# Optimization experiments

Measured on AMD Instinct MI355X. Metric: run time of the kernel, lower is better.

Reference implementation:

```python
import jax, jax.numpy as jnp
import numpy as np

E = 8        # number of sessions (experts)
N = 512      # per-session input width (max units)
P = 512      # n_channels (output width)
F = 100      # max_F time bins
B = 128      # batch of trials
SCALE = 1.0


def setup_inputs() -> dict:
    key = jax.random.key(0)
    kx, ke, k1, k2, k3, k4 = jax.random.split(key, 6)
    x = jax.random.normal(kx, (B, F, N), dtype=jnp.float32)
    eid = jax.random.randint(ke, (B,), 0, E, dtype=jnp.int32)
    # Per-session stitcher Linear(N, 2N) and projector Linear(2N, P), stacked.
    s1 = 1.0 / np.sqrt(N)
    s2 = 1.0 / np.sqrt(2 * N)
    W1 = jax.random.uniform(k1, (E, N, 2 * N), jnp.float32, -s1, s1)
    b1 = jax.random.uniform(k2, (E, 2 * N), jnp.float32, -s1, s1)
    W2 = jax.random.uniform(k3, (E, 2 * N, P), jnp.float32, -s2, s2)
    b2 = jax.random.uniform(k4, (E, P), jnp.float32, -s2, s2)
    return {"x": x, "eid": eid, "W1": W1, "b1": b1, "W2": W2, "b2": b2}


def reference(x, eid, W1, b1, W2, b2):
    # Grouped (per-session) Linear -> Softsign -> Linear, dispatched by eid.
    # Equivalent to the torch loop over unique eids with mask gather/scatter,
    # expressed as a gather of per-sample expert weights + batched matmul.
    w1 = W1[eid]                      # [B, N, 2N]
    stitched = jnp.einsum('bfn,bnh->bfh', x, w1) + b1[eid][:, None, :]
    act = stitched / (1.0 + jnp.abs(stitched))  # Softsign
    act = act * SCALE
    w2 = W2[eid]                      # [B, 2N, P]
    out = jnp.einsum('bfh,bhp->bfp', act, w2) + b2[eid][:, None, :]
    return out                        # [B, F, P]
```

## Files before the change

kernel.cpp:

```cpp
#include <hip/hip_runtime.h>
#include <hip/hip_bf16.h>

#define B_ 128
#define F_ 100
#define N_ 512
#define H_ 1024
#define P_ 512
#define E_ 8

#define BM 128
#define BK 64

typedef __attribute__((ext_vector_type(8))) short bf16x8;
typedef __attribute__((ext_vector_type(4))) float f32x4;

#define GLOAD16(g, l) __builtin_amdgcn_global_load_lds(                      \
    (const __attribute__((address_space(1))) void*)(g),                      \
    (__attribute__((address_space(3))) void*)(l), 16, 0, 0)

static __device__ __forceinline__ short f2bf(float f) {
    __hip_bfloat16 h = __float2bfloat16(f);
    short s;
    __builtin_memcpy(&s, &h, sizeof(s));
    return s;
}

__global__ __launch_bounds__(256) void convert_x(const float* __restrict__ x,
                                                 short* __restrict__ xbf) {
    const int g = blockIdx.x * 256 + threadIdx.x;
    const int col = (g & (N_ / 8 - 1)) * 8;
    const int row = g >> 6;
    const int f = row & 127, b = row >> 7;
    union { short s[8]; uint4 u; } o;
    if (f < F_) {
        const float* xp = x + ((size_t)(b * F_ + f)) * N_ + col;
        const float4 v0 = *(const float4*)(xp);
        const float4 v1 = *(const float4*)(xp + 4);
        o.s[0] = f2bf(v0.x); o.s[1] = f2bf(v0.y);
        o.s[2] = f2bf(v0.z); o.s[3] = f2bf(v0.w);
        o.s[4] = f2bf(v1.x); o.s[5] = f2bf(v1.y);
        o.s[6] = f2bf(v1.z); o.s[7] = f2bf(v1.w);
    } else {
        o.u = make_uint4(0u, 0u, 0u, 0u);
    }
    *(uint4*)(xbf + (size_t)row * N_ + col) = o.u;
}

__global__ __launch_bounds__(256) void transpose_cvt(const float* __restrict__ W,
                                                     short* __restrict__ WT,
                                                     int R, int C) {
    __shared__ float tile[64][65];
    const int e = blockIdx.z;
    const int c0 = blockIdx.x * 64, r0 = blockIdx.y * 64;
    const int t = threadIdx.x;
    const float* Wp = W + (size_t)e * R * C;
    short* WTp = WT + (size_t)e * C * R;
    {
        const int c4 = (t & 15) * 4, r = t >> 4;
#pragma unroll
        for (int p = 0; p < 4; p++) {
            const int row = p * 16 + r;
            const float4 v = *(const float4*)(Wp + (size_t)(r0 + row) * C + c0 + c4);
            tile[row][c4 + 0] = v.x; tile[row][c4 + 1] = v.y;
            tile[row][c4 + 2] = v.z; tile[row][c4 + 3] = v.w;
        }
    }
    __syncthreads();
    {
        const int r8 = (t & 7) * 8, cl = t >> 3;
#pragma unroll
        for (int p = 0; p < 2; p++) {
            const int c = p * 32 + cl;
            union { short s[8]; uint4 u; } o;
#pragma unroll
            for (int j = 0; j < 8; j++) o.s[j] = f2bf(tile[r8 + j][c]);
            *(uint4*)(&WTp[(size_t)(c0 + c) * R + r0 + r8]) = o.u;
        }
    }
}

template <int KDIM, int BN_, bool FIRST>
__global__ __launch_bounds__(256, 4) void gemm_kernel(
    const short* __restrict__ A,
    const short* __restrict__ WT,
    const float* __restrict__ bias,
    const int* __restrict__ eid,
    short* __restrict__ actout,
    float* __restrict__ out)
{
    constexpr int NCOLS = FIRST ? H_ : P_;
    constexpr int NI = BN_ / 32;
    __shared__ short sA[BM * BK];
    __shared__ short sB[BN_ * BK];
    const int b = blockIdx.y;
    const int n0 = blockIdx.x * BN_;
    const int e = eid[b];
    const int t = threadIdx.x;
    const int lane = t & 63, w = t >> 6;
    const int wm = (w >> 1) * 64, wn = (w & 1) * (BN_ / 2);
    const int l15 = lane & 15, quad = lane >> 4;
    const int lr = lane >> 3, lc = (lane & 7) * 8;

    f32x4 acc[4][NI];
#pragma unroll
    for (int mi = 0; mi < 4; mi++)
#pragma unroll
        for (int ni = 0; ni < NI; ni++)
            acc[mi][ni] = (f32x4)(0.0f);

    const short* Ap = A + (size_t)b * BM * KDIM;
    const short* Bp = WT + ((size_t)e * NCOLS + n0) * KDIM;

    for (int k0 = 0; k0 < KDIM; k0 += BK) {
#pragma unroll
        for (int i = 0; i < 4; i++) {
            const int rb = w * 32 + i * 8;
            GLOAD16(Ap + (size_t)(rb + lr) * KDIM + k0 + lc, &sA[rb * BK]);
        }
#pragma unroll
        for (int i = 0; i < BN_ / 32; i++) {
            const int rb = w * (BN_ / 4) + i * 8;
            GLOAD16(Bp + (size_t)(rb + lr) * KDIM + k0 + lc, &sB[rb * BK]);
        }
        __syncthreads();
#pragma unroll
        for (int ks = 0; ks < 2; ks++) {
            bf16x8 af[4], bfr[NI];
#pragma unroll
            for (int mi = 0; mi < 4; mi++)
                af[mi] = *(const bf16x8*)(&sA[(wm + mi * 16 + l15) * BK + ks * 32 + quad * 8]);
#pragma unroll
            for (int ni = 0; ni < NI; ni++)
                bfr[ni] = *(const bf16x8*)(&sB[(wn + ni * 16 + l15) * BK + ks * 32 + quad * 8]);
#pragma unroll
            for (int mi = 0; mi < 4; mi++)
#pragma unroll
                for (int ni = 0; ni < NI; ni++)
                    acc[mi][ni] = __builtin_amdgcn_mfma_f32_16x16x32_bf16(af[mi], bfr[ni], acc[mi][ni], 0, 0, 0);
        }
        __syncthreads();
    }

#pragma unroll
    for (int mi = 0; mi < 4; mi++) {
#pragma unroll
        for (int ni = 0; ni < NI; ni++) {
            const int col = n0 + wn + ni * 16 + l15;
            const float bv = bias[(size_t)e * NCOLS + col];
#pragma unroll
            for (int r = 0; r < 4; r++) {
                const int row = wm + mi * 16 + quad * 4 + r;
                float v = acc[mi][ni][r] + bv;
                if constexpr (FIRST) {
                    v = v / (1.0f + fabsf(v));
                    actout[((size_t)b * BM + row) * H_ + col] = f2bf(v);
                } else {
                    if (row < F_)
                        out[((size_t)b * F_ + row) * P_ + col] = v;
                }
            }
        }
    }
}

extern "C" void kernel_launch(void* const* d_in, const int* in_sizes, int n_in,
                              void* d_out, int out_size, void* d_ws, size_t ws_size,
                              hipStream_t stream) {
    const float* x  = (const float*)d_in[0];
    const int* eid  = (const int*)d_in[1];
    const float* W1 = (const float*)d_in[2];
    const float* b1 = (const float*)d_in[3];
    const float* W2 = (const float*)d_in[4];
    const float* b2 = (const float*)d_in[5];
    float* out = (float*)d_out;

    char* ws = (char*)d_ws;
    short* W1T = (short*)(ws);
    short* W2T = (short*)(ws + (size_t)(8u << 20));
    short* act = (short*)(ws + (size_t)(16u << 20));
    short* xbf = (short*)(ws + (size_t)(48u << 20));

    convert_x<<<dim3((B_ * 128 * N_ / 8) / 256), 256, 0, stream>>>(x, xbf);
    transpose_cvt<<<dim3(H_ / 64, N_ / 64, E_), 256, 0, stream>>>(W1, W1T, N_, H_);
    transpose_cvt<<<dim3(P_ / 64, H_ / 64, E_), 256, 0, stream>>>(W2, W2T, H_, P_);
    gemm_kernel<N_, 128, true><<<dim3(H_ / 128, B_), 256, 0, stream>>>(xbf, W1T, b1, eid, act, nullptr);
    gemm_kernel<H_, 64, false><<<dim3(P_ / 64, B_), 256, 0, stream>>>(act, W2T, b2, eid, nullptr, out);
}
```

Measured before the change: 185.4 us.

## Fuse prep kernels, sort trials by expert, swizzle LDS, trim padded rows

Merges the x conversion and both weight transposes into one launch, which also builds a trial table sorted by expert id. The GEMMs now walk trials in expert order so consecutive blocks share the same weight tiles in cache. LDS reads and writes use an XOR swizzle to avoid bank conflicts, GEMM2 uses a 128-wide N tile, and the bottom waves skip their fourth M-fragment so less work is spent on padded rows (112 instead of 128 per trial). The risk is that A loads for the last trial's rows 100..127 in GEMM1 read past xbf into adjacent workspace, and that the swizzle must match exactly between the global-to-LDS writes and the fragment reads.

```diff
diff --git a/kernel.cpp b/kernel.cpp
--- a/kernel.cpp
+++ b/kernel.cpp
@@ -7,8 +7,7 @@
 #define H_ 1024
 #define P_ 512
 #define E_ 8
-
-#define BM 128
+#define TR_ 112
 #define BK 64
 
 typedef __attribute__((ext_vector_type(8))) short bf16x8;
@@ -25,90 +24,115 @@
     return s;
 }
 
-__global__ __launch_bounds__(256) void convert_x(const float* __restrict__ x,
-                                                 short* __restrict__ xbf) {
-    const int g = blockIdx.x * 256 + threadIdx.x;
-    const int col = (g & (N_ / 8 - 1)) * 8;
-    const int row = g >> 6;
-    const int f = row & 127, b = row >> 7;
-    union { short s[8]; uint4 u; } o;
-    if (f < F_) {
-        const float* xp = x + ((size_t)(b * F_ + f)) * N_ + col;
+__global__ __launch_bounds__(256) void prep(
+    const float* __restrict__ x, const float* __restrict__ W1,
+    const float* __restrict__ W2, const int* __restrict__ eid,
+    short* __restrict__ xbf, short* __restrict__ W1T, short* __restrict__ W2T,
+    int2* __restrict__ ttab) {
+    __shared__ float tile[64][65];
+    __shared__ int scnt[E_], sbase[E_];
+    const int bx = blockIdx.x;
+    const int t = threadIdx.x;
+    if (bx < 3200) {
+        const int g = bx * 256 + t;
+        const int col = (g & 63) * 8;
+        const int row = g >> 6;
+        const float* xp = x + (size_t)row * N_ + col;
         const float4 v0 = *(const float4*)(xp);
         const float4 v1 = *(const float4*)(xp + 4);
+        union { short s[8]; uint4 u; } o;
         o.s[0] = f2bf(v0.x); o.s[1] = f2bf(v0.y);
         o.s[2] = f2bf(v0.z); o.s[3] = f2bf(v0.w);
         o.s[4] = f2bf(v1.x); o.s[5] = f2bf(v1.y);
         o.s[6] = f2bf(v1.z); o.s[7] = f2bf(v1.w);
+        *(uint4*)(xbf + (size_t)row * N_ + col) = o.u;
+    } else if (bx < 5248) {
+        const float* W; short* WT; int R, C, r0, c0, e;
+        if (bx < 4224) {
+            const int idx = bx - 3200;
+            e = idx >> 7; const int i = idx & 127;
+            W = W1; WT = W1T; R = N_; C = H_;
+            r0 = (i >> 4) * 64; c0 = (i & 15) * 64;
+        } else {
+            const int idx = bx - 4224;
+            e = idx >> 7; const int i = idx & 127;
+            W = W2; WT = W2T; R = H_; C = P_;
+            r0 = (i & 15) * 64; c0 = (i >> 4) * 64;
+        }
+        const float* Wp = W + (size_t)e * R * C;
+        short* WTp = WT + (size_t)e * C * R;
+        {
+            const int c4 = (t & 15) * 4, r = t >> 4;
+#pragma unroll
+            for (int p = 0; p < 4; p++) {
+                const int row = p * 16 + r;
+                const float4 v = *(const float4*)(Wp + (size_t)(r0 + row) * C + c0 + c4);
+                tile[row][c4 + 0] = v.x; tile[row][c4 + 1] = v.y;
+                tile[row][c4 + 2] = v.z; tile[row][c4 + 3] = v.w;
+            }
+        }
+        __syncthreads();
+        {
+            const int r8 = (t & 7) * 8, cl = t >> 3;
+#pragma unroll
+            for (int p = 0; p < 2; p++) {
+                const int c = p * 32 + cl;
+                union { short s[8]; uint4 u; } o;
+#pragma unroll
+                for (int j = 0; j < 8; j++) o.s[j] = f2bf(tile[r8 + j][c]);
+                *(uint4*)(&WTp[(size_t)(c0 + c) * R + r0 + r8]) = o.u;
+            }
+        }
     } else {
-        o.u = make_uint4(0u, 0u, 0u, 0u);
+        if (t < E_) scnt[t] = 0;
+        __syncthreads();
+        int my_e = 0;
+        if (t < B_) { my_e = eid[t]; atomicAdd(&scnt[my_e], 1); }
+        __syncthreads();
+        if (t == 0) {
+            int s = 0;
+            for (int i = 0; i < E_; i++) { sbase[i] = s; s += scnt[i]; }
+        }
+        __syncthreads();
+        if (t < B_) {
+            const int pos = atomicAdd(&sbase[my_e], 1);
+            ttab[pos] = make_int2(t, my_e);
+        }
     }
-    *(uint4*)(xbf + (size_t)row * N_ + col) = o.u;
-}
-
-__global__ __launch_bounds__(256) void transpose_cvt(const float* __restrict__ W,
-                                                     short* __restrict__ WT,
-                                                     int R, int C) {
-    __shared__ float tile[64][65];
-    const int e = blockIdx.z;
-    const int c0 = blockIdx.x * 64, r0 = blockIdx.y * 64;
-    const int t = threadIdx.x;
-    const float* Wp = W + (size_t)e * R * C;
-    short* WTp = WT + (size_t)e * C * R;
-    {
-        const int c4 = (t & 15) * 4, r = t >> 4;
-#pragma unroll
-        for (int p = 0; p < 4; p++) {
-            const int row = p * 16 + r;
-            const float4 v = *(const float4*)(Wp + (size_t)(r0 + row) * C + c0 + c4);
-            tile[row][c4 + 0] = v.x; tile[row][c4 + 1] = v.y;
-            tile[row][c4 + 2] = v.z; tile[row][c4 + 3] = v.w;
-        }
-    }
-    __syncthreads();
-    {
-        const int r8 = (t & 7) * 8, cl = t >> 3;
-#pragma unroll
-        for (int p = 0; p < 2; p++) {
-            const int c = p * 32 + cl;
-            union { short s[8]; uint4 u; } o;
-#pragma unroll
-            for (int j = 0; j < 8; j++) o.s[j] = f2bf(tile[r8 + j][c]);
-            *(uint4*)(&WTp[(size_t)(c0 + c) * R + r0 + r8]) = o.u;
-        }
-    }
-}
-
-template <int KDIM, int BN_, bool FIRST>
+}
+
+template <int KDIM, bool FIRST>
 __global__ __launch_bounds__(256, 4) void gemm_kernel(
     const short* __restrict__ A,
     const short* __restrict__ WT,
     const float* __restrict__ bias,
-    const int* __restrict__ eid,
+    const int2* __restrict__ ttab,
     short* __restrict__ actout,
     float* __restrict__ out)
 {
     constexpr int NCOLS = FIRST ? H_ : P_;
-    constexpr int NI = BN_ / 32;
-    __shared__ short sA[BM * BK];
-    __shared__ short sB[BN_ * BK];
-    const int b = blockIdx.y;
-    const int n0 = blockIdx.x * BN_;
-    const int e = eid[b];
+    __shared__ short sA[128 * BK];
+    __shared__ short sB[128 * BK];
+    const int slot = (blockIdx.x & 7) * 16 + (blockIdx.x >> 3);
+    const int2 te = ttab[slot];
+    const int trial = te.x, e = te.y;
+    const int n0 = blockIdx.y * 128;
     const int t = threadIdx.x;
     const int lane = t & 63, w = t >> 6;
-    const int wm = (w >> 1) * 64, wn = (w & 1) * (BN_ / 2);
+    const int wm = (w >> 1) * 64, wn = (w & 1) * 64;
+    const int MI = (w >> 1) ? 3 : 4;
     const int l15 = lane & 15, quad = lane >> 4;
-    const int lr = lane >> 3, lc = (lane & 7) * 8;
-
-    f32x4 acc[4][NI];
+    const int lr = lane >> 3;
+    const int lc = (((lane & 7) ^ lr) * 8);
+
+    f32x4 acc[4][4];
 #pragma unroll
     for (int mi = 0; mi < 4; mi++)
 #pragma unroll
-        for (int ni = 0; ni < NI; ni++)
+        for (int ni = 0; ni < 4; ni++)
             acc[mi][ni] = (f32x4)(0.0f);
 
-    const short* Ap = A + (size_t)b * BM * KDIM;
+    const short* Ap = A + (size_t)trial * (FIRST ? F_ : TR_) * KDIM;
     const short* Bp = WT + ((size_t)e * NCOLS + n0) * KDIM;
 
     for (int k0 = 0; k0 < KDIM; k0 += BK) {
@@ -118,33 +142,31 @@
             GLOAD16(Ap + (size_t)(rb + lr) * KDIM + k0 + lc, &sA[rb * BK]);
         }
 #pragma unroll
-        for (int i = 0; i < BN_ / 32; i++) {
-            const int rb = w * (BN_ / 4) + i * 8;
+        for (int i = 0; i < 4; i++) {
+            const int rb = w * 32 + i * 8;
             GLOAD16(Bp + (size_t)(rb + lr) * KDIM + k0 + lc, &sB[rb * BK]);
         }
         __syncthreads();
 #pragma unroll
         for (int ks = 0; ks < 2; ks++) {
-            bf16x8 af[4], bfr[NI];
-#pragma unroll
-            for (int mi = 0; mi < 4; mi++)
-                af[mi] = *(const bf16x8*)(&sA[(wm + mi * 16 + l15) * BK + ks * 32 + quad * 8]);
-#pragma unroll
-            for (int ni = 0; ni < NI; ni++)
-                bfr[ni] = *(const bf16x8*)(&sB[(wn + ni * 16 + l15) * BK + ks * 32 + quad * 8]);
-#pragma unroll
-            for (int mi = 0; mi < 4; mi++)
-#pragma unroll
-                for (int ni = 0; ni < NI; ni++)
+            const int sw = (((ks * 4 + quad) ^ (l15 & 7)) * 8);
+            bf16x8 af[4], bfr[4];
+            for (int mi = 0; mi < MI; mi++)
+                af[mi] = *(const bf16x8*)(&sA[(wm + mi * 16 + l15) * BK + sw]);
+#pragma unroll
+            for (int ni = 0; ni < 4; ni++)
+                bfr[ni] = *(const bf16x8*)(&sB[(wn + ni * 16 + l15) * BK + sw]);
+            for (int mi = 0; mi < MI; mi++)
+#pragma unroll
+                for (int ni = 0; ni < 4; ni++)
                     acc[mi][ni] = __builtin_amdgcn_mfma_f32_16x16x32_bf16(af[mi], bfr[ni], acc[mi][ni], 0, 0, 0);
         }
         __syncthreads();
     }
 
-#pragma unroll
-    for (int mi = 0; mi < 4; mi++) {
-#pragma unroll
-        for (int ni = 0; ni < NI; ni++) {
+    for (int mi = 0; mi < MI; mi++) {
+#pragma unroll
+        for (int ni = 0; ni < 4; ni++) {
             const int col = n0 + wn + ni * 16 + l15;
             const float bv = bias[(size_t)e * NCOLS + col];
 #pragma unroll
@@ -153,10 +175,10 @@
                 float v = acc[mi][ni][r] + bv;
                 if constexpr (FIRST) {
                     v = v / (1.0f + fabsf(v));
-                    actout[((size_t)b * BM + row) * H_ + col] = f2bf(v);
+                    actout[((size_t)trial * TR_ + row) * H_ + col] = f2bf(v);
                 } else {
                     if (row < F_)
-                        out[((size_t)b * F_ + row) * P_ + col] = v;
+                        out[((size_t)trial * F_ + row) * P_ + col] = v;
                 }
             }
         }
@@ -178,11 +200,10 @@
     short* W1T = (short*)(ws);
     short* W2T = (short*)(ws + (size_t)(8u << 20));
     short* act = (short*)(ws + (size_t)(16u << 20));
-    short* xbf = (short*)(ws + (size_t)(48u << 20));
-
-    convert_x<<<dim3((B_ * 128 * N_ / 8) / 256), 256, 0, stream>>>(x, xbf);
-    transpose_cvt<<<dim3(H_ / 64, N_ / 64, E_), 256, 0, stream>>>(W1, W1T, N_, H_);
-    transpose_cvt<<<dim3(P_ / 64, H_ / 64, E_), 256, 0, stream>>>(W2, W2T, H_, P_);
-    gemm_kernel<N_, 128, true><<<dim3(H_ / 128, B_), 256, 0, stream>>>(xbf, W1T, b1, eid, act, nullptr);
-    gemm_kernel<H_, 64, false><<<dim3(P_ / 64, B_), 256, 0, stream>>>(act, W2T, b2, eid, nullptr, out);
-}
+    short* xbf = (short*)(ws + (size_t)(47u << 20));
+    int2* ttab = (int2*)(ws + (size_t)(62u << 20));
+
+    prep<<<dim3(5249), 256, 0, stream>>>(x, W1, W2, eid, xbf, W1T, W2T, ttab);
+    gemm_kernel<N_, true><<<dim3(B_, H_ / 128), 256, 0, stream>>>(xbf, W1T, b1, ttab, act, nullptr);
+    gemm_kernel<H_, false><<<dim3(B_, P_ / 128), 256, 0, stream>>>(act, W2T, b2, ttab, nullptr, out);
+}
```

Result: slower. 724.0 us (+290.4%).
